# Optimization experiments

Hardware: AMD Instinct MI355X
Metric: run time of the kernel (lower is better)

The kernel has to match this reference:

```python
import jax, jax.numpy as jnp
import numpy as np

B, L, V = 16, 2048, 64


def setup_inputs() -> dict:
    key = jax.random.key(0)
    k1, k2, k3, k4 = jax.random.split(key, 4)
    idx = jax.random.randint(k1, (B, L), 0, V)                      # tokens
    Wq_w = jax.random.normal(k2, (V, V), jnp.float32) * 0.02         # nn.Linear weight
    Wv_w = jax.random.normal(k3, (V, V), jnp.float32) * 0.02 + np.float32(np.e)  # Wv.weight (+e init)
    v_emb = jax.random.normal(k4, (L, 1), jnp.float32) * 0.02        # nn.Embedding(length, 1)
    return {"idx": idx, "Wq_w": Wq_w, "Wv_w": Wv_w, "v_emb": v_emb}


def reference(idx, Wq_w, Wv_w, v_emb):
    Lx = v_emb.shape[0]
    Vx = Wq_w.shape[0]
    # e = one_hot token embedding, [B, L, V]
    e = jax.nn.one_hot(idx, Vx, dtype=jnp.float32)
    i = jnp.arange(Lx)
    # pos[i, j] = max(i - j, 0); learned relative-position score table [L, L]
    pos = jnp.maximum(i[:, None] - i[None, :], 0)
    pos_embd = v_emb[pos, 0]
    causal = i[:, None] >= i[None, :]                                # tril mask
    # Attention block 1: scores are the learned position table (no QK^T)
    attn1 = jax.nn.softmax(jnp.where(causal, pos_embd, -jnp.inf), axis=-1)  # [L, L]
    l1 = jnp.einsum('ts,bsv->btv', attn1, e)                         # [B, L, V]
    # Attention block 2: Wq(e) @ l1^T, masked softmax, attn @ e * scalar
    q = jnp.einsum('btv,uv->btu', e, Wq_w)                           # F.linear: e @ Wq^T
    scores = jnp.einsum('btv,bsv->bts', q, l1)                       # [B, L, L]
    attn2 = jax.nn.softmax(jnp.where(causal, scores, -jnp.inf), axis=-1)
    l2 = jnp.einsum('bts,bsv->btv', attn2, e) * Wv_w[0, 0]           # logits [B, L, V]
    return l2
```

## Files before the change

kernel.cpp:

```cpp
#include <hip/hip_runtime.h>


#define LSEQ 2048
#define NB 16
#define NV 64
#define CS 64
#define NC (LSEQ / CS)

typedef __attribute__((ext_vector_type(8))) short bf16x8;
typedef __attribute__((ext_vector_type(4))) float f32x4;

__device__ __forceinline__ unsigned short f2bf(float f) {
  unsigned int u = __float_as_uint(f);
  return (unsigned short)((u + 0x7FFFu + ((u >> 16) & 1u)) >> 16);
}

__global__ __launch_bounds__(256) void k_gather(const int* __restrict__ idx,
                                                const float* __restrict__ Wq,
                                                const float* __restrict__ v_emb,
                                                unsigned short* __restrict__ Agr,
                                                unsigned short* __restrict__ Ebf,
                                                float* __restrict__ S) {
  const int b = blockIdx.x >> 4;
  const int tile = blockIdx.x & 15;
  const int w = threadIdx.x >> 6;
  const int lane = threadIdx.x & 63;

  if (blockIdx.x == 0 && threadIdx.x < 64) {
    const int base = lane * 32;
    float e[32];
    float run = 0.f;
#pragma unroll
    for (int i = 0; i < 32; ++i) { e[i] = expf(v_emb[base + i]); run += e[i]; }
    float incl = run;
#pragma unroll
    for (int d = 1; d < 64; d <<= 1) {
      float up = __shfl_up(incl, d);
      if (lane >= d) incl += up;
    }
    float acc = incl - run;
#pragma unroll
    for (int i = 0; i < 32; ++i) {
      acc += e[i];
      Ebf[base + i] = f2bf(e[i]);
      S[base + i] = acc;
    }
  }

  const int k8base = tile * 16 + w * 4;
#pragma unroll
  for (int r = 0; r < 4; ++r) {
    const int k8 = k8base + r;
    unsigned short v[8];
#pragma unroll
    for (int j = 0; j < 8; ++j) {
      const int ii = idx[b * LSEQ + (2047 - (k8 * 8 + j))];
      v[j] = f2bf(Wq[ii * 64 + lane]);
    }
    uint4 st;
    st.x = (unsigned int)v[0] | ((unsigned int)v[1] << 16);
    st.y = (unsigned int)v[2] | ((unsigned int)v[3] << 16);
    st.z = (unsigned int)v[4] | ((unsigned int)v[5] << 16);
    st.w = (unsigned int)v[6] | ((unsigned int)v[7] << 16);
    *(uint4*)(Agr + ((size_t)(b * 256 + k8) * 64 + lane) * 8) = st;
  }
}

__global__ __launch_bounds__(256) void k_gemm(const unsigned short* __restrict__ Agr,
                                              const unsigned short* __restrict__ Ebf,
                                              const float* __restrict__ S,
                                              float* __restrict__ P) {
  __shared__ unsigned short GL0[2208];
  __shared__ unsigned short GL1[2176];
  __shared__ float red[16][64];
  __shared__ float red2[16][64];

  const int b  = blockIdx.y;
  const int bn = 63 - (int)blockIdx.x;
  const int n0 = bn * 32;
  const int tid = threadIdx.x;
  const int w = tid >> 6;
  const int lane = tid & 63;
  const int quad = lane >> 4;
  const int lm = lane & 15;
  const int nsub = w & 1;
  const int kh = w >> 1;

  for (int i = tid; i < 2208; i += 256) {
    const int e = i - 127;
    GL0[i] = (e >= 0 && e < LSEQ) ? Ebf[e] : (unsigned short)0;
  }
  for (int i = tid; i < 2176; i += 256) {
    const int e = i + 1 - 127;
    GL1[i] = (e >= 0 && e < LSEQ) ? Ebf[e] : (unsigned short)0;
  }
  __syncthreads();

  f32x4 acc[4];
#pragma unroll
  for (int mt = 0; mt < 4; ++mt) acc[mt] = (f32x4){0.f, 0.f, 0.f, 0.f};

  const int nbase = n0 + nsub * 16;
  const int sbase = nbase + lm - 1920;
  const int kstart = 2048 - (n0 + 32);
  const int iters = bn + 1;
  const unsigned short* __restrict__ abase = Agr + (size_t)b * 256 * 64 * 8;

  union AF { uint4 u; bf16x8 v; };
  union BF { unsigned int u[4]; bf16x8 v; };
  AF a[3][4];
  BF bb[3];

#define LOAD_FRAGS(J_, SL) do {                                             \
    const int k_ = kstart + (kh + 2 * (J_)) * 32;                           \
    const int kq8_ = (k_ >> 3) + quad;                                      \
    const unsigned short* ab_ = abase + ((size_t)kq8_ * 64 + lm) * 8;       \
    a[SL][0].u = *(const uint4*)(ab_ + 0 * 128);                            \
    a[SL][1].u = *(const uint4*)(ab_ + 1 * 128);                            \
    a[SL][2].u = *(const uint4*)(ab_ + 2 * 128);                            \
    a[SL][3].u = *(const uint4*)(ab_ + 3 * 128);                            \
    const int s_ = sbase + k_ + quad * 8;                                   \
    const unsigned int* gb_ = (s_ & 1) ? (const unsigned int*)GL1           \
                                       : (const unsigned int*)GL0;          \
    const int off_ = s_ >> 1;                                               \
    bb[SL].u[0] = gb_[off_ + 0]; bb[SL].u[1] = gb_[off_ + 1];               \
    bb[SL].u[2] = gb_[off_ + 2]; bb[SL].u[3] = gb_[off_ + 3];               \
  } while (0)

#define MFMA4(SL) do {                                                      \
    acc[0] = __builtin_amdgcn_mfma_f32_16x16x32_bf16(a[SL][0].v, bb[SL].v, acc[0], 0, 0, 0); \
    acc[1] = __builtin_amdgcn_mfma_f32_16x16x32_bf16(a[SL][1].v, bb[SL].v, acc[1], 0, 0, 0); \
    acc[2] = __builtin_amdgcn_mfma_f32_16x16x32_bf16(a[SL][2].v, bb[SL].v, acc[2], 0, 0, 0); \
    acc[3] = __builtin_amdgcn_mfma_f32_16x16x32_bf16(a[SL][3].v, bb[SL].v, acc[3], 0, 0, 0); \
  } while (0)

  const int J = (iters > kh) ? ((iters - kh + 1) >> 1) : 0;
  if (J > 0) {
    LOAD_FRAGS(0, 0);
    if (J > 1) LOAD_FRAGS(1, 1);
    int j = 0;
    while (true) {
      if (j + 2 < J) LOAD_FRAGS(j + 2, 2);
      MFMA4(0);
      if (++j >= J) break;
      if (j + 2 < J) LOAD_FRAGS(j + 2, 0);
      MFMA4(1);
      if (++j >= J) break;
      if (j + 2 < J) LOAD_FRAGS(j + 2, 1);
      MFMA4(2);
      if (++j >= J) break;
    }
  }
#undef LOAD_FRAGS
#undef MFMA4

  if (kh == 1) {
    float (*rd)[64] = nsub ? red2 : red;
#pragma unroll
    for (int mt = 0; mt < 4; ++mt)
#pragma unroll
      for (int r = 0; r < 4; ++r) rd[mt * 4 + r][lane] = acc[mt][r];
  }
  __syncthreads();
  if (kh == 0) {
    float (*rd)[64] = nsub ? red2 : red;
#pragma unroll
    for (int mt = 0; mt < 4; ++mt)
#pragma unroll
      for (int r = 0; r < 4; ++r) acc[mt][r] += rd[mt * 4 + r][lane];

    const float sinv = 1.0f / S[nbase + lm];
#pragma unroll
    for (int mt = 0; mt < 4; ++mt) {
#pragma unroll
      for (int r = 0; r < 4; ++r) {
        const int c = mt * 16 + quad * 4 + r;
        P[((size_t)(b * 64 + c)) * LSEQ + nbase + lm] = __expf(acc[mt][r] * sinv);
      }
    }
  }
}

__global__ __launch_bounds__(256) void k_chist(const int* __restrict__ idx,
                                               const float* __restrict__ P,
                                               float* __restrict__ hist) {
  __shared__ float bins[4][64];
  const int ch = blockIdx.x;
  const int cg = blockIdx.y;
  const int b  = blockIdx.z;
  const int w = threadIdx.x >> 6;
  const int lane = threadIdx.x & 63;
  const int c = cg * 4 + w;
  const int bc = b * 64 + c;
  const int s0 = ch * 64;

  const float p = P[(size_t)bc * LSEQ + s0 + lane];
  const int ii = idx[b * LSEQ + s0 + lane];
  bins[w][lane] = 0.f;
  __syncthreads();
  atomicAdd(&bins[w][ii], p);
  __syncthreads();
  hist[((size_t)bc * NC + ch) * 64 + lane] = bins[w][lane];
}

__global__ __launch_bounds__(256) void k_emit(const int* __restrict__ idx,
                                              const float* __restrict__ P,
                                              const float* __restrict__ hist,
                                              const float* __restrict__ Wv,
                                              float* __restrict__ out) {
  __shared__ float bins[4][64];
  const int tg = blockIdx.x;
  const int b  = blockIdx.y;
  const int w = threadIdx.x >> 6;
  const int lane = threadIdx.x & 63;
  const int t = tg * 4 + w;
  const int c = idx[b * LSEQ + t];
  const int bc = b * 64 + c;
  const int ch = t >> 6;
  const int s0 = ch * 64;
  const int rel = t - s0;

  float p = P[(size_t)bc * LSEQ + s0 + lane];
  const int ii = idx[b * LSEQ + s0 + lane];
  p = (lane <= rel) ? p : 0.f;
  bins[w][lane] = 0.f;
  __syncthreads();
  atomicAdd(&bins[w][ii], p);
  __syncthreads();

  const float* __restrict__ h = hist + (size_t)bc * NC * 64 + lane;
  float t0 = 0.f, t1 = 0.f, t2 = 0.f, t3 = 0.f;
  int ch2 = 0;
  for (; ch2 + 4 <= ch; ch2 += 4) {
    t0 += h[(ch2 + 0) * 64];
    t1 += h[(ch2 + 1) * 64];
    t2 += h[(ch2 + 2) * 64];
    t3 += h[(ch2 + 3) * 64];
  }
  for (; ch2 < ch; ++ch2) t0 += h[ch2 * 64];
  float bin = bins[w][lane] + ((t0 + t1) + (t2 + t3));

  float z = bin;
#pragma unroll
  for (int d = 1; d < 64; d <<= 1) z += __shfl_xor(z, d);
  out[((size_t)(b * LSEQ + t)) * 64 + lane] = Wv[0] * bin / z;
}

extern "C" void kernel_launch(void* const* d_in, const int* in_sizes, int n_in,
                              void* d_out, int out_size, void* d_ws, size_t ws_size,
                              hipStream_t stream) {
  const int* idx     = (const int*)d_in[0];
  const float* Wq    = (const float*)d_in[1];
  const float* Wv    = (const float*)d_in[2];
  const float* v_emb = (const float*)d_in[3];
  float* out = (float*)d_out;

  float* S = (float*)d_ws;
  float* P = S + LSEQ;
  float* hist = P + (size_t)NB * NV * LSEQ;
  unsigned short* Ebf = (unsigned short*)(hist + (size_t)NB * NV * NC * 64);
  unsigned short* Agr = Ebf + LSEQ;

  k_gather<<<NB * 16, 256, 0, stream>>>(idx, Wq, v_emb, Agr, Ebf, S);
  k_gemm<<<dim3(64, NB), 256, 0, stream>>>(Agr, Ebf, S, P);
  k_chist<<<dim3(NC, 16, NB), 256, 0, stream>>>(idx, P, hist);
  k_emit<<<dim3(LSEQ / 4, NB), 256, 0, stream>>>(idx, P, hist, Wv, out);
}
```

Baseline: 124.9 us.

## Drop chunk-histogram kernel; emit scans full prefix per token directly

Removes the k_chist pass and its hist workspace. Each k_emit wavefront now accumulates the whole causal prefix of P into shared bins with LDS atomics instead of summing precomputed per-chunk histograms. It also trims the k_gemm LDS staging loop to fill only the window that block needs. This saves one launch and the hist write/read, but emit work now grows linearly with position, giving O(L) loads and atomics per token. The __syncthreads between zeroing and the atomics was replaced by a __threadfence_block, which is probably only safe because each wave uses its own bins row.

```diff
diff --git a/kernel.cpp b/kernel.cpp
--- a/kernel.cpp
+++ b/kernel.cpp
@@ -4,8 +4,6 @@
 #define LSEQ 2048
 #define NB 16
 #define NV 64
-#define CS 64
-#define NC (LSEQ / CS)
 
 typedef __attribute__((ext_vector_type(8))) short bf16x8;
 typedef __attribute__((ext_vector_type(4))) float f32x4;
@@ -86,13 +84,14 @@
   const int nsub = w & 1;
   const int kh = w >> 1;
 
-  for (int i = tid; i < 2208; i += 256) {
-    const int e = i - 127;
-    GL0[i] = (e >= 0 && e < LSEQ) ? Ebf[e] : (unsigned short)0;
-  }
-  for (int i = tid; i < 2176; i += 256) {
-    const int e = i + 1 - 127;
-    GL1[i] = (e >= 0 && e < LSEQ) ? Ebf[e] : (unsigned short)0;
+  {
+    const int wend = n0 + 160;
+    for (int i = 96 + tid; i < wend; i += 256) {
+      const int e0 = i - 127;
+      const int e1 = i - 126;
+      GL0[i] = (e0 >= 0 && e0 < LSEQ) ? Ebf[e0] : (unsigned short)0;
+      GL1[i] = (e1 >= 0 && e1 < LSEQ) ? Ebf[e1] : (unsigned short)0;
+    }
   }
   __syncthreads();
 
@@ -181,31 +180,8 @@
   }
 }
 
-__global__ __launch_bounds__(256) void k_chist(const int* __restrict__ idx,
-                                               const float* __restrict__ P,
-                                               float* __restrict__ hist) {
-  __shared__ float bins[4][64];
-  const int ch = blockIdx.x;
-  const int cg = blockIdx.y;
-  const int b  = blockIdx.z;
-  const int w = threadIdx.x >> 6;
-  const int lane = threadIdx.x & 63;
-  const int c = cg * 4 + w;
-  const int bc = b * 64 + c;
-  const int s0 = ch * 64;
-
-  const float p = P[(size_t)bc * LSEQ + s0 + lane];
-  const int ii = idx[b * LSEQ + s0 + lane];
-  bins[w][lane] = 0.f;
-  __syncthreads();
-  atomicAdd(&bins[w][ii], p);
-  __syncthreads();
-  hist[((size_t)bc * NC + ch) * 64 + lane] = bins[w][lane];
-}
-
 __global__ __launch_bounds__(256) void k_emit(const int* __restrict__ idx,
                                               const float* __restrict__ P,
-                                              const float* __restrict__ hist,
                                               const float* __restrict__ Wv,
                                               float* __restrict__ out) {
   __shared__ float bins[4][64];
@@ -217,28 +193,35 @@
   const int c = idx[b * LSEQ + t];
   const int bc = b * 64 + c;
   const int ch = t >> 6;
-  const int s0 = ch * 64;
-  const int rel = t - s0;
-
-  float p = P[(size_t)bc * LSEQ + s0 + lane];
-  const int ii = idx[b * LSEQ + s0 + lane];
-  p = (lane <= rel) ? p : 0.f;
+  const int rel = t & 63;
+
+  const float* __restrict__ prow = P + (size_t)bc * LSEQ;
+  const int* __restrict__ irow = idx + b * LSEQ;
+
   bins[w][lane] = 0.f;
-  __syncthreads();
-  atomicAdd(&bins[w][ii], p);
-  __syncthreads();
-
-  const float* __restrict__ h = hist + (size_t)bc * NC * 64 + lane;
-  float t0 = 0.f, t1 = 0.f, t2 = 0.f, t3 = 0.f;
-  int ch2 = 0;
-  for (; ch2 + 4 <= ch; ch2 += 4) {
-    t0 += h[(ch2 + 0) * 64];
-    t1 += h[(ch2 + 1) * 64];
-    t2 += h[(ch2 + 2) * 64];
-    t3 += h[(ch2 + 3) * 64];
-  }
-  for (; ch2 < ch; ++ch2) t0 += h[ch2 * 64];
-  float bin = bins[w][lane] + ((t0 + t1) + (t2 + t3));
+
+  int g = 0;
+  for (; g + 4 <= ch; g += 4) {
+    const float p0 = prow[(g + 0) * 64 + lane]; const int i0 = irow[(g + 0) * 64 + lane];
+    const float p1 = prow[(g + 1) * 64 + lane]; const int i1 = irow[(g + 1) * 64 + lane];
+    const float p2 = prow[(g + 2) * 64 + lane]; const int i2 = irow[(g + 2) * 64 + lane];
+    const float p3 = prow[(g + 3) * 64 + lane]; const int i3 = irow[(g + 3) * 64 + lane];
+    atomicAdd(&bins[w][i0], p0);
+    atomicAdd(&bins[w][i1], p1);
+    atomicAdd(&bins[w][i2], p2);
+    atomicAdd(&bins[w][i3], p3);
+  }
+  for (; g < ch; ++g) {
+    const float p0 = prow[g * 64 + lane]; const int i0 = irow[g * 64 + lane];
+    atomicAdd(&bins[w][i0], p0);
+  }
+  {
+    float p0 = prow[ch * 64 + lane]; const int i0 = irow[ch * 64 + lane];
+    p0 = (lane <= rel) ? p0 : 0.f;
+    atomicAdd(&bins[w][i0], p0);
+  }
+  __threadfence_block();
+  const float bin = bins[w][lane];
 
   float z = bin;
 #pragma unroll
@@ -257,12 +240,10 @@
 
   float* S = (float*)d_ws;
   float* P = S + LSEQ;
-  float* hist = P + (size_t)NB * NV * LSEQ;
-  unsigned short* Ebf = (unsigned short*)(hist + (size_t)NB * NV * NC * 64);
+  unsigned short* Ebf = (unsigned short*)(P + (size_t)NB * NV * LSEQ);
   unsigned short* Agr = Ebf + LSEQ;
 
   k_gather<<<NB * 16, 256, 0, stream>>>(idx, Wq, v_emb, Agr, Ebf, S);
   k_gemm<<<dim3(64, NB), 256, 0, stream>>>(Agr, Ebf, S, P);
-  k_chist<<<dim3(NC, 16, NB), 256, 0, stream>>>(idx, P, hist);
-  k_emit<<<dim3(LSEQ / 4, NB), 256, 0, stream>>>(idx, P, hist, Wv, out);
-}
+  k_emit<<<dim3(LSEQ / 4, NB), 256, 0, stream>>>(idx, P, Wv, out);
+}
```

New measurement: 285.3 us. 128% more time.
